# Performance work log

Hardware: AMD Instinct MI355X
Metric: run time of the kernel (lower is better)

The kernel has to match this reference:

```python
import jax, jax.numpy as jnp
import numpy as np

N = 8192       # num_nodes
DEG = 16       # edges per node
E = N * DEG    # num_edges
F = 128        # num_features
R = 20         # num_rbf_features
L = 3          # num_message_passing_layers
CUT = 3.0      # cutoff_dist


def setup_inputs() -> dict:
    key = jax.random.key(0)
    ks = jax.random.split(key, 18)
    atoms = jax.random.randint(ks[0], (N,), 1, 119)
    # every node appears as a destination exactly DEG times -> bincount > 0
    idx_i = jnp.repeat(jnp.arange(N), DEG)
    idx_j = jax.random.randint(ks[1], (E,), 0, N)
    raw = jax.random.normal(ks[2], (E, 3), jnp.float32)
    rel_dir = raw / jnp.linalg.norm(raw, axis=-1, keepdims=True)
    rel_dist = jax.random.uniform(ks[3], (E,), jnp.float32, 0.1, CUT - 1e-3)
    emb = (jax.random.normal(ks[4], (119, F), jnp.float32) / np.sqrt(F)).at[0].set(0.0)
    def w(k, shape, fan_in):
        return jax.random.normal(k, shape, jnp.float32) / np.sqrt(fan_in)
    return {
        'atoms': atoms, 'idx_i': idx_i, 'idx_j': idx_j,
        'rel_dir': rel_dir, 'rel_dist': rel_dist, 'emb': emb,
        'msg_w1': w(ks[5], (L, F, F), F), 'msg_b1': jnp.zeros((L, F), jnp.float32),
        'msg_w2': w(ks[6], (L, F, 3 * F), F), 'msg_b2': jnp.zeros((L, 3 * F), jnp.float32),
        'rbf_w': w(ks[7], (L, R, 3 * F), R), 'rbf_b': jnp.zeros((L, 3 * F), jnp.float32),
        'Uw': w(ks[8], (L, F, F), F), 'Vw': w(ks[9], (L, F, F), F),
        'upd_w1': w(ks[10], (L, 2 * F, F), 2 * F), 'upd_b1': jnp.zeros((L, F), jnp.float32),
        'upd_w2': w(ks[11], (L, F, 3 * F), F), 'upd_b2': jnp.zeros((L, 3 * F), jnp.float32),
    }


def painn_forward(atoms, idx_i, idx_j, rel_dir, rel_dist, emb,
                  msg_w1, msg_b1, msg_w2, msg_b2, rbf_w, rbf_b,
                  Uw, Vw, upd_w1, upd_b1, upd_w2, upd_b2):
    silu = jax.nn.silu
    # cosine cutoff and sinusoidal RBF features of edge distances
    cut = 0.5 * (jnp.cos(jnp.pi * rel_dist / CUT) + 1.0)               # [E]
    n = jnp.arange(1, R + 1, dtype=rel_dist.dtype)
    rbf = jnp.sin(n * jnp.pi * rel_dist[:, None] / CUT) / rel_dist[:, None]  # [E,R]

    s = emb[atoms]                                   # [N,F]
    v = jnp.zeros((N, F, 3), s.dtype)                # [N,F,3]
    counts = jax.ops.segment_sum(jnp.ones(E, s.dtype), idx_i, num_segments=N)  # bincount

    for l in range(L):
        # ---- message block ----
        phi = silu(s @ msg_w1[l] + msg_b1[l]) @ msg_w2[l] + msg_b2[l]  # [N,3F]
        W = (rbf @ rbf_w[l] + rbf_b[l]) * cut[:, None]                 # [E,3F]
        phi_W = phi[idx_j] * W                                         # [E,3F]
        p_vv, p_ss, p_vs = jnp.split(phi_W, 3, axis=-1)
        ds = jax.ops.segment_sum(p_ss, idx_i, num_segments=N) / counts[:, None]
        ve = v[idx_j] * p_vv[..., None] + p_vs[..., None] * rel_dir[:, None, :]  # [E,F,3]
        dv = jax.ops.segment_sum(ve, idx_i, num_segments=N) / counts[:, None, None]
        s = s + ds
        v = v + dv
        # ---- update block ----
        Uv = jnp.einsum('nfc,fg->ngc', v, Uw[l])       # [N,F,3]
        Vv = jnp.einsum('nfc,fg->ngc', v, Vw[l])       # [N,F,3]
        a_in = jnp.concatenate([jnp.linalg.norm(Vv, axis=-1), s], axis=-1)  # [N,2F]
        a = silu(a_in @ upd_w1[l] + upd_b1[l]) @ upd_w2[l] + upd_b2[l]      # [N,3F]
        a_vv, a_sv, a_ss = jnp.split(a, 3, axis=-1)
        s = s + a_ss + a_sv * jnp.sum(Uv * Vv, axis=-1)
        v = v + Uv * a_vv[..., None]
    return s, v


def reference(atoms, idx_i, idx_j, rel_dir, rel_dist, emb,
              msg_w1, msg_b1, msg_w2, msg_b2, rbf_w, rbf_b,
              Uw, Vw, upd_w1, upd_b1, upd_w2, upd_b2):
    return painn_forward(atoms, idx_i, idx_j, rel_dir, rel_dist, emb,
                         msg_w1, msg_b1, msg_w2, msg_b2, rbf_w, rbf_b,
                         Uw, Vw, upd_w1, upd_b1, upd_w2, upd_b2)
```

## Files before the change

### kernel.cpp

```cpp
#include <hip/hip_runtime.h>
#include <hip/hip_fp16.h>

#define N_NODES 8192
#define DEG     16
#define NEDGE   (N_NODES*DEG)
#define F       128
#define F3      384
#define RBF     20
#define NLAYER  3
#define NF      (N_NODES*F)
#define PI_F    3.14159265358979f

typedef unsigned short u16;
typedef __bf16 bf16x8 __attribute__((ext_vector_type(8)));
typedef float  f32x4  __attribute__((ext_vector_type(4)));

__device__ __forceinline__ float bf2f(u16 u){ return __uint_as_float(((unsigned)u)<<16); }
__device__ __forceinline__ u16 f2bf(float f){
  unsigned x = __float_as_uint(f);
  unsigned r = (x + 0x7FFFu + ((x>>16)&1u)) >> 16;
  return (u16)r;
}
__device__ __forceinline__ float lo_bf(unsigned u){ return __uint_as_float(u<<16); }
__device__ __forceinline__ float hi_bf(unsigned u){ return __uint_as_float(u & 0xFFFF0000u); }
__device__ __forceinline__ float silu_f(float x){ return x / (1.f + __expf(-x)); }
__device__ __forceinline__ float ldsrc(const void* src, int i, int bf){
  return bf ? bf2f(((const u16*)src)[i]) : ((const float*)src)[i];
}
__device__ __forceinline__ unsigned packh2(float a, float b){
  return (unsigned)__half_as_ushort(__float2half(a)) |
         ((unsigned)__half_as_ushort(__float2half(b)) << 16);
}
__device__ __forceinline__ __half2 u2h2(unsigned u){ return __builtin_bit_cast(__half2, u); }

__global__ void k_detect(const u16* __restrict__ rd, int* __restrict__ flag){
  if (threadIdx.x == 0 && blockIdx.x == 0){
    int ok = 1;
    for (int i = 0; i < 128; i++){
      float v = bf2f(rd[2*i]);
      if (!(v > 0.01f && v < 4.0f)) { ok = 0; break; }
    }
    *flag = ok;
  }
}

__device__ __forceinline__ void splitw(const void* src, u16* bh, u16* bl,
                                       int i, int K, int Ncol, int bf){
  int kn = K*Ncol; int l = i/kn; int r = i - l*kn; int k = r/Ncol; int n = r - k*Ncol;
  float w = ldsrc(src, i, bf);
  u16 h = f2bf(w);
  size_t o = (size_t)l*kn + (size_t)n*K + k;
  bh[o] = h; bl[o] = f2bf(w - bf2f(h));
}

__global__ __launch_bounds__(256) void k_prep(
    const void* mb1, const void* mb2, const void* b1, const void* b2,
    const void* rw,  const void* rb,
    const void* mw1, const void* mw2, const void* w1, const void* w2,
    const void* Uw,  const void* Vw,
    const void* dist, const void* dirv, const int* __restrict__ idxj,
    const int* __restrict__ atoms, const void* __restrict__ emb,
    float* c_mb1, float* c_mb2, float* c_b1, float* c_b2,
    unsigned* rwp2,
    u16* mw1h, u16* mw1l, u16* mw2h, u16* mw2l, u16* w1h, u16* w1l,
    u16* w2h, u16* w2l, u16* uvh, u16* uvl,
    uint4* edata,
    float* s, u16* s_h, u16* s_l,
    u16* p0h, u16* p0l, u16* bufA16, u16* bufB16,
    const int* __restrict__ flag){
  int i = blockIdx.x*256 + threadIdx.x;
  int bf = *flag;
  const int S0=NLAYER*F, S1=NLAYER*F3, S2=NLAYER*F, S3=NLAYER*F3;
  const int S4=NLAYER*11*F3;
  const int S5=NLAYER*F*F, S6=NLAYER*F*F3, S7=NLAYER*2*F*F, S8=NLAYER*F*F3, S9=NLAYER*256*F;
  if (i < S0){ c_mb1[i]=ldsrc(mb1,i,bf); return; } i-=S0;
  if (i < S1){ c_mb2[i]=ldsrc(mb2,i,bf); return; } i-=S1;
  if (i < S2){ c_b1[i] =ldsrc(b1, i,bf); return; } i-=S2;
  if (i < S3){ c_b2[i] =ldsrc(b2, i,bf); return; } i-=S3;
  if (i < S4){
    int l = i/(11*F3); int r = i - l*(11*F3); int r2 = r/F3; int col = r - r2*F3;
    float w0, w1v;
    if (r2 < 10){
      w0  = ldsrc(rw, (l*RBF + 2*r2  )*F3 + col, bf);
      w1v = ldsrc(rw, (l*RBF + 2*r2+1)*F3 + col, bf);
    } else {
      w0  = ldsrc(rb, l*F3 + col, bf);
      w1v = 0.f;
    }
    rwp2[i] = packh2(w0, w1v);
    return;
  } i-=S4;
  if (i < S5){ splitw(mw1, mw1h, mw1l, i, F,   F,  bf); return; } i-=S5;
  if (i < S6){ splitw(mw2, mw2h, mw2l, i, F,   F3, bf); return; } i-=S6;
  if (i < S7){ splitw(w1,  w1h,  w1l,  i, 2*F, F,  bf); return; } i-=S7;
  if (i < S8){ splitw(w2,  w2h,  w2l,  i, F,   F3, bf); return; } i-=S8;
  if (i < S9){
    int l=i/(256*F); int r=i-l*(256*F); int n=r>>7; int k=r&127;
    int si=(l*F+k)*F+(n&127);
    float w = ldsrc((n<128)?Uw:Vw, si, bf);
    u16 h=f2bf(w); uvh[i]=h; uvl[i]=f2bf(w-bf2f(h));
    return;
  } i-=S9;
  if (i < NEDGE){
    int e = i;
    float d = ldsrc(dist, e, bf);
    float cut = 0.5f*(cosf(PI_F*d*(1.f/3.f)) + 1.0f);
    float ic = cut/d;
    unsigned o[16];
    #pragma unroll
    for (int r2=0;r2<10;r2++){
      float s0 = sinf((2*r2+1)*PI_F*d*(1.f/3.f))*ic;
      float s1 = sinf((2*r2+2)*PI_F*d*(1.f/3.f))*ic;
      o[r2] = packh2(s0, s1);
    }
    o[10] = packh2(cut, 0.f);
    o[11] = __float_as_uint(ldsrc(dirv, e*3+0, bf));
    o[12] = __float_as_uint(ldsrc(dirv, e*3+1, bf));
    o[13] = __float_as_uint(ldsrc(dirv, e*3+2, bf));
    o[14] = (unsigned)idxj[e];
    o[15] = 0;
    uint4* dst = edata + (size_t)e*4;
    dst[0] = make_uint4(o[0],o[1],o[2],o[3]);
    dst[1] = make_uint4(o[4],o[5],o[6],o[7]);
    dst[2] = make_uint4(o[8],o[9],o[10],o[11]);
    dst[3] = make_uint4(o[12],o[13],o[14],o[15]);
    return;
  } i-=NEDGE;
  if (i < NF){
    int n = i >> 7, f = i & 127;
    float sv = ldsrc(emb, atoms[n]*F + f, bf);
    s[i] = sv;
    u16 hb = f2bf(sv); s_h[i] = hb; s_l[i] = f2bf(sv - bf2f(hb));
    p0h[i]=0; p0h[NF+i]=0; p0h[2*(size_t)NF+i]=0;
    p0l[i]=0; p0l[NF+i]=0; p0l[2*(size_t)NF+i]=0;
    bufA16[(size_t)i*4+2]=0; bufA16[(size_t)i*4+3]=0;
    bufB16[(size_t)i*2+1]=0;
  }
}
#define PREP_TOTAL (NLAYER*(F+F3+F+F3+11*F3+F*F+F*F3+2*F*F+F*F3+256*F) + NEDGE + NF)

__global__ __launch_bounds__(256) void k_msg(const u16* __restrict__ s_h,
                                             const u16* __restrict__ s_l,
                                             const u16* __restrict__ w1h_,
                                             const u16* __restrict__ w1l_,
                                             const u16* __restrict__ w2h_,
                                             const u16* __restrict__ w2l_,
                                             const float* __restrict__ b1,
                                             const float* __restrict__ b2,
                                             u16* __restrict__ bufA16,
                                             u16* __restrict__ bufB16){
  __shared__ u16 Ah[16*136], Al[16*136];
  __shared__ u16 Hh[16*136], Hl[16*136];
  __shared__ u16 Bh[64*136], Bl[64*136];
  int t = threadIdx.x, lane = t&63, w = t>>6;
  int row0 = blockIdx.x<<4;
  int l15 = lane&15, q8 = (lane>>4)<<3, qrow = (lane>>4)<<2;

  #pragma unroll
  for (int q=0;q<2;q++){
    int id = t + 256*q; int pl = id>>8, rem = id&255, r = rem>>4, c = (rem&15)<<3;
    *(uint4*)((pl?Al:Ah)+r*136+c) = *(const uint4*)((pl?s_l:s_h) + (size_t)(row0+r)*F + c);
  }

  for (int cg=0;cg<2;cg++){
    __syncthreads();
    #pragma unroll
    for (int q=0;q<8;q++){
      int id = t + 256*q; int pl = id>>10, rem = id&1023, r = rem>>4, c = (rem&15)<<3;
      *(uint4*)((pl?Bl:Bh)+r*136+c) = *(const uint4*)((pl?w1l_:w1h_) + (size_t)(cg*64+r)*F + c);
    }
    __syncthreads();
    f32x4 acc; acc[0]=0;acc[1]=0;acc[2]=0;acc[3]=0;
    #pragma unroll
    for (int k0=0;k0<F;k0+=32){
      bf16x8 a_h = *(const bf16x8*)&Ah[l15*136 + k0 + q8];
      bf16x8 a_l = *(const bf16x8*)&Al[l15*136 + k0 + q8];
      bf16x8 b_h = *(const bf16x8*)&Bh[(w*16+l15)*136 + k0 + q8];
      bf16x8 b_l = *(const bf16x8*)&Bl[(w*16+l15)*136 + k0 + q8];
      acc = __builtin_amdgcn_mfma_f32_16x16x32_bf16(a_h, b_h, acc, 0,0,0);
      acc = __builtin_amdgcn_mfma_f32_16x16x32_bf16(a_h, b_l, acc, 0,0,0);
      acc = __builtin_amdgcn_mfma_f32_16x16x32_bf16(a_l, b_h, acc, 0,0,0);
    }
    int col = cg*64 + w*16 + l15;
    float bb = b1[col];
    #pragma unroll
    for (int r=0;r<4;r++){
      float val = silu_f(acc[r] + bb);
      u16 hb = f2bf(val);
      Hh[(qrow+r)*136 + col] = hb;
      Hl[(qrow+r)*136 + col] = f2bf(val - bf2f(hb));
    }
  }

  for (int cg=0;cg<6;cg++){
    __syncthreads();
    #pragma unroll
    for (int q=0;q<8;q++){
      int id = t + 256*q; int pl = id>>10, rem = id&1023, r = rem>>4, c = (rem&15)<<3;
      *(uint4*)((pl?Bl:Bh)+r*136+c) = *(const uint4*)((pl?w2l_:w2h_) + (size_t)(cg*64+r)*F + c);
    }
    __syncthreads();
    f32x4 acc; acc[0]=0;acc[1]=0;acc[2]=0;acc[3]=0;
    #pragma unroll
    for (int k0=0;k0<F;k0+=32){
      bf16x8 a_h = *(const bf16x8*)&Hh[l15*136 + k0 + q8];
      bf16x8 a_l = *(const bf16x8*)&Hl[l15*136 + k0 + q8];
      bf16x8 b_h = *(const bf16x8*)&Bh[(w*16+l15)*136 + k0 + q8];
      bf16x8 b_l = *(const bf16x8*)&Bl[(w*16+l15)*136 + k0 + q8];
      acc = __builtin_amdgcn_mfma_f32_16x16x32_bf16(a_h, b_h, acc, 0,0,0);
      acc = __builtin_amdgcn_mfma_f32_16x16x32_bf16(a_h, b_l, acc, 0,0,0);
      acc = __builtin_amdgcn_mfma_f32_16x16x32_bf16(a_l, b_h, acc, 0,0,0);
    }
    int gc = cg*64 + w*16 + l15;
    float bb = b2[gc];
    #pragma unroll
    for (int r=0;r<4;r++){
      int grow = row0 + qrow + r;
      u16 v = f2bf(acc[r] + bb);
      size_t rowo = (size_t)grow*F;
      if (gc < F)        bufA16[(rowo + gc)*4 + 0]     = v;
      else if (gc < 2*F) bufA16[(rowo + gc - F)*4 + 1] = v;
      else               bufB16[(rowo + gc - 2*F)*2]   = v;
    }
  }
}

__global__ __launch_bounds__(256) void k_agg(const uint4* __restrict__ ed_g,
                                             const uint2* __restrict__ bufA,
                                             const unsigned* __restrict__ bufB,
                                             const unsigned* __restrict__ rwp2,
                                             const u16* __restrict__ vi_h,
                                             const u16* __restrict__ vi_l,
                                             u16* __restrict__ vo_h,
                                             u16* __restrict__ vo_l,
                                             float* __restrict__ s,
                                             u16* __restrict__ s_h,
                                             u16* __restrict__ s_l){
  __shared__ uint4 ed4[128];
  int t = threadIdx.x;
  int half = t >> 7, f = t & 127;

  __half2 rw2[3][11];
  #pragma unroll
  for (int r2=0;r2<11;r2++){
    rw2[0][r2] = u2h2(rwp2[r2*F3 + f]);
    rw2[1][r2] = u2h2(rwp2[r2*F3 + F + f]);
    rw2[2][r2] = u2h2(rwp2[r2*F3 + 2*F + f]);
  }

  int nA = blockIdx.x * 2;
  if (t < 128) ed4[t] = ed_g[(size_t)nA*64 + t];
  __syncthreads();

  int n = nA + half;
  int base = half*64;
  float ds=0.f, dv0=0.f, dv1=0.f, dv2=0.f;

  int j0 = (int)(ed4[base+3].z & (N_NODES-1));
  uint2    pa = bufA[(size_t)j0*F + f];
  unsigned pb = bufB[(size_t)j0*F + f];
  for (int el=0;el<DEG;el++){
    uint2 cpa = pa; unsigned cpb = pb;
    if (el+1 < DEG){
      int j1 = (int)(ed4[base+(el+1)*4+3].z & (N_NODES-1));
      pa = bufA[(size_t)j1*F + f];
      pb = bufB[(size_t)j1*F + f];
    }
    uint4 q0 = ed4[base+el*4+0];
    uint4 q1 = ed4[base+el*4+1];
    uint4 q2 = ed4[base+el*4+2];
    uint4 q3 = ed4[base+el*4+3];
    __half2 rc[11] = {u2h2(q0.x),u2h2(q0.y),u2h2(q0.z),u2h2(q0.w),
                      u2h2(q1.x),u2h2(q1.y),u2h2(q1.z),u2h2(q1.w),
                      u2h2(q2.x),u2h2(q2.y),u2h2(q2.z)};
    __half2 a0 = __hmul2(rc[0], rw2[0][0]);
    __half2 a1 = __hmul2(rc[0], rw2[1][0]);
    __half2 a2 = __hmul2(rc[0], rw2[2][0]);
    #pragma unroll
    for (int r2=1;r2<11;r2++){
      a0 = __hfma2(rc[r2], rw2[0][r2], a0);
      a1 = __hfma2(rc[r2], rw2[1][r2], a1);
      a2 = __hfma2(rc[r2], rw2[2][r2], a2);
    }
    float Wvv = __low2float(a0) + __high2float(a0);
    float Wss = __low2float(a1) + __high2float(a1);
    float Wvs = __low2float(a2) + __high2float(a2);
    float pvv = Wvv*lo_bf(cpa.x), pss = Wss*hi_bf(cpa.x), pvs = Wvs*lo_bf(cpb);
    ds += pss;
    dv0 += lo_bf(cpa.y)*pvv + pvs*__uint_as_float(q2.w);
    dv1 += hi_bf(cpa.y)*pvv + pvs*__uint_as_float(q3.x);
    dv2 += hi_bf(cpb)  *pvv + pvs*__uint_as_float(q3.y);
  }
  size_t i = (size_t)n*F + f;
  const float inv = 1.f/DEG;
  float sv = s[i] + ds*inv;
  s[i] = sv;
  { u16 hb = f2bf(sv); s_h[i] = hb; s_l[i] = f2bf(sv - bf2f(hb)); }
  float o0 = bf2f(vi_h[i])            + bf2f(vi_l[i])            + dv0*inv;
  float o1 = bf2f(vi_h[NF+i])         + bf2f(vi_l[NF+i])         + dv1*inv;
  float o2 = bf2f(vi_h[2*(size_t)NF+i]) + bf2f(vi_l[2*(size_t)NF+i]) + dv2*inv;
  u16 h0=f2bf(o0), h1=f2bf(o1), h2=f2bf(o2);
  vo_h[i]=h0; vo_h[NF+i]=h1; vo_h[2*(size_t)NF+i]=h2;
  vo_l[i]=f2bf(o0-bf2f(h0)); vo_l[NF+i]=f2bf(o1-bf2f(h1)); vo_l[2*(size_t)NF+i]=f2bf(o2-bf2f(h2));
}

__global__ __launch_bounds__(256) void k_uvdot(const u16* __restrict__ voh,
                                               const u16* __restrict__ vol,
                                               const u16* __restrict__ Bh_g,
                                               const u16* __restrict__ Bl_g,
                                               const float* __restrict__ s,
                                               float* __restrict__ uvF,
                                               float* __restrict__ dot,
                                               u16* __restrict__ ai_h,
                                               u16* __restrict__ ai_l){
  __shared__ u16 Ah[32*40], Al[32*40], BUh[64*40], BUl[64*40], BVh[64*40], BVl[64*40];
  int t = threadIdx.x;
  int row0 = blockIdx.y<<5, c0 = blockIdx.x<<6;
  int lane = t&63, w = t>>6;
  int qr = (w>>1)<<4, qc = (w&1)<<5;
  int l15 = lane&15, q8 = (lane>>4)<<3;
  int qrow = (lane>>4)<<2;
  int ap = t>>7, arem = t&127, ar = arem>>2, ac = (arem&3)<<3;
  f32x4 dA[2], nA2[2];
  dA[0][0]=0;dA[0][1]=0;dA[0][2]=0;dA[0][3]=0; dA[1]=dA[0];
  nA2[0]=dA[0]; nA2[1]=dA[0];

  for (int c=0;c<3;c++){
    f32x4 aU[2], aV[2];
    aU[0][0]=0;aU[0][1]=0;aU[0][2]=0;aU[0][3]=0; aU[1]=aU[0];
    aV[0]=aU[0]; aV[1]=aU[0];
    const u16* Asrc = (ap ? vol : voh) + (size_t)c*NF + (size_t)(row0+ar)*F + ac;
    u16* Adst = (ap ? Al : Ah) + ar*40 + ac;
    for (int k0=0;k0<F;k0+=32){
      *(uint4*)Adst = *(const uint4*)(Asrc + k0);
      #pragma unroll
      for (int q=0;q<4;q++){
        int idx = t + 256*q;
        int bp = idx>>8, rem = idx&255, br = rem>>2, bc = (rem&3)<<3;
        int grow = ((bp>>1) ? 128 : 0) + c0 + br;
        const u16* Bsrc = ((bp&1) ? Bl_g : Bh_g) + (size_t)grow*F + k0 + bc;
        u16* Bdst;
        if (bp==0) Bdst = BUh; else if (bp==1) Bdst = BUl; else if (bp==2) Bdst = BVh; else Bdst = BVl;
        *(uint4*)(Bdst + br*40 + bc) = *(const uint4*)Bsrc;
      }
      __syncthreads();
      bf16x8 a_h = *(const bf16x8*)&Ah[(qr+l15)*40 + q8];
      bf16x8 a_l = *(const bf16x8*)&Al[(qr+l15)*40 + q8];
      #pragma unroll
      for (int nt=0;nt<2;nt++){
        int off = (qc+nt*16+l15)*40 + q8;
        bf16x8 bu_h = *(const bf16x8*)&BUh[off];
        bf16x8 bu_l = *(const bf16x8*)&BUl[off];
        bf16x8 bv_h = *(const bf16x8*)&BVh[off];
        bf16x8 bv_l = *(const bf16x8*)&BVl[off];
        aU[nt] = __builtin_amdgcn_mfma_f32_16x16x32_bf16(a_h, bu_h, aU[nt], 0,0,0);
        aU[nt] = __builtin_amdgcn_mfma_f32_16x16x32_bf16(a_h, bu_l, aU[nt], 0,0,0);
        aU[nt] = __builtin_amdgcn_mfma_f32_16x16x32_bf16(a_l, bu_h, aU[nt], 0,0,0);
        aV[nt] = __builtin_amdgcn_mfma_f32_16x16x32_bf16(a_h, bv_h, aV[nt], 0,0,0);
        aV[nt] = __builtin_amdgcn_mfma_f32_16x16x32_bf16(a_h, bv_l, aV[nt], 0,0,0);
        aV[nt] = __builtin_amdgcn_mfma_f32_16x16x32_bf16(a_l, bv_h, aV[nt], 0,0,0);
      }
      __syncthreads();
    }
    #pragma unroll
    for (int nt=0;nt<2;nt++){
      int gcol = c0 + qc + nt*16 + l15;
      #pragma unroll
      for (int r=0;r<4;r++){
        int grow = row0 + qr + qrow + r;
        float u = aU[nt][r], v = aV[nt][r];
        dA[nt][r] += u*v;
        nA2[nt][r] += v*v;
        uvF[(size_t)c*NF + (size_t)grow*F + gcol] = u;
      }
    }
  }
  #pragma unroll
  for (int nt=0;nt<2;nt++){
    int gcol = c0 + qc + nt*16 + l15;
    #pragma unroll
    for (int r=0;r<4;r++){
      int grow = row0 + qr + qrow + r;
      dot[(size_t)grow*F + gcol] = dA[nt][r];
      float vn = sqrtf(nA2[nt][r]);
      float sv = s[(size_t)grow*F + gcol];
      size_t b = (size_t)grow*256 + gcol;
      u16 h0 = f2bf(vn), h1 = f2bf(sv);
      ai_h[b] = h0;     ai_l[b] = f2bf(vn - bf2f(h0));
      ai_h[b+128] = h1; ai_l[b+128] = f2bf(sv - bf2f(h1));
    }
  }
}

__global__ __launch_bounds__(256) void k_upd(const u16* __restrict__ ai_h,
                                             const u16* __restrict__ ai_l,
                                             const u16* __restrict__ w1h_,
                                             const u16* __restrict__ w1l_,
                                             const u16* __restrict__ w2h_,
                                             const u16* __restrict__ w2l_,
                                             const float* __restrict__ b1,
                                             const float* __restrict__ b2,
                                             const float* __restrict__ dot,
                                             const float* __restrict__ uvF,
                                             float* __restrict__ s,
                                             u16* __restrict__ s_h,
                                             u16* __restrict__ s_l,
                                             u16* __restrict__ v_h,
                                             u16* __restrict__ v_l,
                                             u16* __restrict__ bufA16,
                                             u16* __restrict__ bufB16,
                                             float* __restrict__ out){
  __shared__ u16 Ah[16*264], Al[16*264];
  __shared__ u16 Hh[16*136], Hl[16*136];
  __shared__ u16 Bh[64*136], Bl[64*136];
  __shared__ __half aLDS[16*392];
  int t = threadIdx.x, lane = t&63, w = t>>6;
  int row0 = blockIdx.x<<4;
  int l15 = lane&15, q8 = (lane>>4)<<3, qrow = (lane>>4)<<2;

  #pragma unroll
  for (int q=0;q<4;q++){
    int id = t + 256*q; int pl = id>>9, rem = id&511, r = rem>>5, c = (rem&31)<<3;
    *(uint4*)((pl?Al:Ah)+r*264+c) = *(const uint4*)((pl?ai_l:ai_h) + (size_t)(row0+r)*256 + c);
  }

  for (int cg=0;cg<2;cg++){
    f32x4 acc; acc[0]=0;acc[1]=0;acc[2]=0;acc[3]=0;
    for (int kc=0;kc<4;kc++){
      __syncthreads();
      #pragma unroll
      for (int q=0;q<4;q++){
        int id = t + 256*q; int pl = id>>9, rem = id&511, r = rem>>3, c = (rem&7)<<3;
        *(uint4*)((pl?Bl:Bh)+r*136+c) =
            *(const uint4*)((pl?w1l_:w1h_) + (size_t)(cg*64+r)*256 + kc*64 + c);
      }
      __syncthreads();
      #pragma unroll
      for (int ks=0;ks<64;ks+=32){
        bf16x8 a_h = *(const bf16x8*)&Ah[l15*264 + kc*64 + ks + q8];
        bf16x8 a_l = *(const bf16x8*)&Al[l15*264 + kc*64 + ks + q8];
        bf16x8 b_h = *(const bf16x8*)&Bh[(w*16+l15)*136 + ks + q8];
        bf16x8 b_l = *(const bf16x8*)&Bl[(w*16+l15)*136 + ks + q8];
        acc = __builtin_amdgcn_mfma_f32_16x16x32_bf16(a_h, b_h, acc, 0,0,0);
        acc = __builtin_amdgcn_mfma_f32_16x16x32_bf16(a_h, b_l, acc, 0,0,0);
        acc = __builtin_amdgcn_mfma_f32_16x16x32_bf16(a_l, b_h, acc, 0,0,0);
      }
    }
    int col = cg*64 + w*16 + l15;
    float bb = b1[col];
    #pragma unroll
    for (int r=0;r<4;r++){
      float val = silu_f(acc[r] + bb);
      u16 hb = f2bf(val);
      Hh[(qrow+r)*136 + col] = hb;
      Hl[(qrow+r)*136 + col] = f2bf(val - bf2f(hb));
    }
  }

  for (int cg=0;cg<6;cg++){
    __syncthreads();
    #pragma unroll
    for (int q=0;q<8;q++){
      int id = t + 256*q; int pl = id>>10, rem = id&1023, r = rem>>4, c = (rem&15)<<3;
      *(uint4*)((pl?Bl:Bh)+r*136+c) = *(const uint4*)((pl?w2l_:w2h_) + (size_t)(cg*64+r)*F + c);
    }
    __syncthreads();
    f32x4 acc; acc[0]=0;acc[1]=0;acc[2]=0;acc[3]=0;
    #pragma unroll
    for (int k0=0;k0<F;k0+=32){
      bf16x8 a_h = *(const bf16x8*)&Hh[l15*136 + k0 + q8];
      bf16x8 a_l = *(const bf16x8*)&Hl[l15*136 + k0 + q8];
      bf16x8 b_h = *(const bf16x8*)&Bh[(w*16+l15)*136 + k0 + q8];
      bf16x8 b_l = *(const bf16x8*)&Bl[(w*16+l15)*136 + k0 + q8];
      acc = __builtin_amdgcn_mfma_f32_16x16x32_bf16(a_h, b_h, acc, 0,0,0);
      acc = __builtin_amdgcn_mfma_f32_16x16x32_bf16(a_h, b_l, acc, 0,0,0);
      acc = __builtin_amdgcn_mfma_f32_16x16x32_bf16(a_l, b_h, acc, 0,0,0);
    }
    int gc = cg*64 + w*16 + l15;
    float bb = b2[gc];
    #pragma unroll
    for (int r=0;r<4;r++)
      aLDS[(qrow+r)*392 + gc] = __float2half(acc[r] + bb);
  }
  __syncthreads();

  int f = t & 127, rh = (t>>7)*8;
  #pragma unroll
  for (int e=0;e<8;e++){
    int r = rh + e;
    int grow = row0 + r;
    size_t i = (size_t)grow*F + f;
    float avv = __half2float(aLDS[r*392 + f]);
    float asv = __half2float(aLDS[r*392 + F + f]);
    float ass = __half2float(aLDS[r*392 + 2*F + f]);
    float sv = s[i] + ass + asv*dot[i];
    s[i] = sv;
    u16 hb = f2bf(sv); s_h[i] = hb; s_l[i] = f2bf(sv - bf2f(hb));
    float nv0 = bf2f(v_h[i])              + bf2f(v_l[i])              + uvF[i]*avv;
    float nv1 = bf2f(v_h[NF+i])           + bf2f(v_l[NF+i])           + uvF[NF+i]*avv;
    float nv2 = bf2f(v_h[2*(size_t)NF+i]) + bf2f(v_l[2*(size_t)NF+i]) + uvF[2*(size_t)NF+i]*avv;
    u16 h0=f2bf(nv0), h1=f2bf(nv1), h2=f2bf(nv2);
    v_h[i]=h0; v_h[NF+i]=h1; v_h[2*(size_t)NF+i]=h2;
    v_l[i]=f2bf(nv0-bf2f(h0)); v_l[NF+i]=f2bf(nv1-bf2f(h1)); v_l[2*(size_t)NF+i]=f2bf(nv2-bf2f(h2));
    bufA16[(size_t)i*4+2] = h0; bufA16[(size_t)i*4+3] = h1;
    bufB16[(size_t)i*2+1] = h2;
    if (out){
      out[i] = sv;
      out[NF + (size_t)i*3 + 0] = nv0;
      out[NF + (size_t)i*3 + 1] = nv1;
      out[NF + (size_t)i*3 + 2] = nv2;
    }
  }
}

extern "C" void kernel_launch(void* const* d_in, const int* in_sizes, int n_in,
                              void* d_out, int out_size, void* d_ws, size_t ws_size,
                              hipStream_t stream) {
  const int* atoms   = (const int*)d_in[0];
  const int* idxj    = (const int*)d_in[2];

  float* W = (float*)d_ws;
  size_t off = 64;
  int* flag = (int*)d_ws;
  #define ALLOCF(name, cnt) float* name = W+off; off += (((cnt)+63)&~(size_t)63)
  #define ALLOCU(name, cnt) u16* name = (u16*)(W+off); off += ((((cnt)+1)/2+63)&~(size_t)63)
  ALLOCF(c_mb1, NLAYER*F);
  ALLOCF(c_mb2, NLAYER*F3);
  ALLOCF(c_b1,  NLAYER*F);
  ALLOCF(c_b2,  NLAYER*F3);
  unsigned* c_rwp2 = (unsigned*)(W+off); off += ((NLAYER*11*F3+63)&~(size_t)63);
  uint4* edata = (uint4*)(W+off); off += (size_t)NEDGE*16;
  ALLOCU(w_mw1h, NLAYER*F*F);   ALLOCU(w_mw1l, NLAYER*F*F);
  ALLOCU(w_mw2h, NLAYER*F*F3);  ALLOCU(w_mw2l, NLAYER*F*F3);
  ALLOCU(w_uvh,  NLAYER*256*F); ALLOCU(w_uvl,  NLAYER*256*F);
  ALLOCU(w_w1h,  NLAYER*F*256); ALLOCU(w_w1l,  NLAYER*F*256);
  ALLOCU(w_w2h,  NLAYER*F*F3);  ALLOCU(w_w2l,  NLAYER*F*F3);
  uint2* bufA = (uint2*)(W+off); off += (size_t)2*NF;
  unsigned* bufB = (unsigned*)(W+off); off += (size_t)NF;
  ALLOCU(p0h, (size_t)3*NF); ALLOCU(p0l, (size_t)3*NF);
  ALLOCU(p1h, (size_t)3*NF); ALLOCU(p1l, (size_t)3*NF);
  ALLOCU(s_h,  NF); ALLOCU(s_l,  NF);
  ALLOCU(ai_h, (size_t)2*NF); ALLOCU(ai_l, (size_t)2*NF);
  ALLOCF(s,    NF);
  ALLOCF(uvF,  (size_t)3*NF);
  ALLOCF(dotb, NF);

  k_detect<<<1, 64, 0, stream>>>((const u16*)d_in[4], flag);
  k_prep<<<(PREP_TOTAL+255)/256, 256, 0, stream>>>(
      d_in[7], d_in[9], d_in[15], d_in[17],
      d_in[10], d_in[11],
      d_in[6], d_in[8], d_in[14], d_in[16],
      d_in[12], d_in[13],
      d_in[4], d_in[3], idxj,
      atoms, d_in[5],
      c_mb1, c_mb2, c_b1, c_b2, c_rwp2,
      w_mw1h, w_mw1l, w_mw2h, w_mw2l, w_w1h, w_w1l,
      w_w2h, w_w2l, w_uvh, w_uvl, edata,
      s, s_h, s_l, p0h, p0l, (u16*)bufA, (u16*)bufB, flag);

  for (int l=0; l<NLAYER; l++){
    u16* vih = (l & 1) ? p1h : p0h;
    u16* vil = (l & 1) ? p1l : p0l;
    u16* voh = (l & 1) ? p0h : p1h;
    u16* vol = (l & 1) ? p0l : p1l;
    k_msg<<<N_NODES/16, 256, 0, stream>>>(
        s_h, s_l,
        w_mw1h + (size_t)l*F*F,  w_mw1l + (size_t)l*F*F,
        w_mw2h + (size_t)l*F*F3, w_mw2l + (size_t)l*F*F3,
        c_mb1 + (size_t)l*F, c_mb2 + (size_t)l*F3,
        (u16*)bufA, (u16*)bufB);
    k_agg<<<N_NODES/2, 256, 0, stream>>>(
        edata, bufA, bufB, c_rwp2 + (size_t)l*11*F3,
        vih, vil, voh, vol, s, s_h, s_l);
    k_uvdot<<<dim3(2, N_NODES/32), 256, 0, stream>>>(
        voh, vol, w_uvh + (size_t)l*256*F, w_uvl + (size_t)l*256*F,
        s, uvF, dotb, ai_h, ai_l);
    k_upd<<<N_NODES/16, 256, 0, stream>>>(
        ai_h, ai_l,
        w_w1h + (size_t)l*F*256, w_w1l + (size_t)l*F*256,
        w_w2h + (size_t)l*F*F3,  w_w2l + (size_t)l*F*F3,
        c_b1 + (size_t)l*F, c_b2 + (size_t)l*F3,
        dotb, uvF, s, s_h, s_l, voh, vol,
        (u16*)bufA, (u16*)bufB,
        (l == NLAYER-1) ? (float*)d_out : nullptr);
  }
}
```

Baseline: 388.5 us.

## Compute RBF edge filters with MFMA into LDS instead of per-thread half2 FMAs

```diff
diff --git a/kernel.cpp b/kernel.cpp
--- a/kernel.cpp
+++ b/kernel.cpp
@@ -27,11 +27,6 @@
 __device__ __forceinline__ float ldsrc(const void* src, int i, int bf){
   return bf ? bf2f(((const u16*)src)[i]) : ((const float*)src)[i];
 }
-__device__ __forceinline__ unsigned packh2(float a, float b){
-  return (unsigned)__half_as_ushort(__float2half(a)) |
-         ((unsigned)__half_as_ushort(__float2half(b)) << 16);
-}
-__device__ __forceinline__ __half2 u2h2(unsigned u){ return __builtin_bit_cast(__half2, u); }
 
 __global__ void k_detect(const u16* __restrict__ rd, int* __restrict__ flag){
   if (threadIdx.x == 0 && blockIdx.x == 0){
@@ -61,35 +56,23 @@
     const void* dist, const void* dirv, const int* __restrict__ idxj,
     const int* __restrict__ atoms, const void* __restrict__ emb,
     float* c_mb1, float* c_mb2, float* c_b1, float* c_b2,
-    unsigned* rwp2,
     u16* mw1h, u16* mw1l, u16* mw2h, u16* mw2l, u16* w1h, u16* w1l,
     u16* w2h, u16* w2l, u16* uvh, u16* uvl,
-    uint4* edata,
+    u16* rwB,
+    u16* ed_rc,
+    uint4* ed2,
     float* s, u16* s_h, u16* s_l,
     u16* p0h, u16* p0l, u16* bufA16, u16* bufB16,
     const int* __restrict__ flag){
   int i = blockIdx.x*256 + threadIdx.x;
   int bf = *flag;
   const int S0=NLAYER*F, S1=NLAYER*F3, S2=NLAYER*F, S3=NLAYER*F3;
-  const int S4=NLAYER*11*F3;
   const int S5=NLAYER*F*F, S6=NLAYER*F*F3, S7=NLAYER*2*F*F, S8=NLAYER*F*F3, S9=NLAYER*256*F;
+  const int SB=NLAYER*24*64*8;
   if (i < S0){ c_mb1[i]=ldsrc(mb1,i,bf); return; } i-=S0;
   if (i < S1){ c_mb2[i]=ldsrc(mb2,i,bf); return; } i-=S1;
   if (i < S2){ c_b1[i] =ldsrc(b1, i,bf); return; } i-=S2;
   if (i < S3){ c_b2[i] =ldsrc(b2, i,bf); return; } i-=S3;
-  if (i < S4){
-    int l = i/(11*F3); int r = i - l*(11*F3); int r2 = r/F3; int col = r - r2*F3;
-    float w0, w1v;
-    if (r2 < 10){
-      w0  = ldsrc(rw, (l*RBF + 2*r2  )*F3 + col, bf);
-      w1v = ldsrc(rw, (l*RBF + 2*r2+1)*F3 + col, bf);
-    } else {
-      w0  = ldsrc(rb, l*F3 + col, bf);
-      w1v = 0.f;
-    }
-    rwp2[i] = packh2(w0, w1v);
-    return;
-  } i-=S4;
   if (i < S5){ splitw(mw1, mw1h, mw1l, i, F,   F,  bf); return; } i-=S5;
   if (i < S6){ splitw(mw2, mw2h, mw2l, i, F,   F3, bf); return; } i-=S6;
   if (i < S7){ splitw(w1,  w1h,  w1l,  i, 2*F, F,  bf); return; } i-=S7;
@@ -101,29 +84,35 @@
     u16 h=f2bf(w); uvh[i]=h; uvl[i]=f2bf(w-bf2f(h));
     return;
   } i-=S9;
+  if (i < SB){
+    int l = i/12288; int r = i - l*12288;
+    int nt = r>>9; int rem = r&511; int lane = rem>>3; int j = rem&7;
+    int k = ((lane>>4)<<3) + j; int n = nt*16 + (lane&15);
+    float v;
+    if (k < RBF)       v = ldsrc(rw, (l*RBF + k)*F3 + n, bf);
+    else if (k == RBF) v = ldsrc(rb, l*F3 + n, bf);
+    else               v = 0.f;
+    rwB[i] = f2bf(v);
+    return;
+  } i-=SB;
   if (i < NEDGE){
-    int e = i;
+    int e = i; int n = e>>4; int el = e&15;
     float d = ldsrc(dist, e, bf);
     float cut = 0.5f*(cosf(PI_F*d*(1.f/3.f)) + 1.0f);
     float ic = cut/d;
-    unsigned o[16];
-    #pragma unroll
-    for (int r2=0;r2<10;r2++){
-      float s0 = sinf((2*r2+1)*PI_F*d*(1.f/3.f))*ic;
-      float s1 = sinf((2*r2+2)*PI_F*d*(1.f/3.f))*ic;
-      o[r2] = packh2(s0, s1);
-    }
-    o[10] = packh2(cut, 0.f);
-    o[11] = __float_as_uint(ldsrc(dirv, e*3+0, bf));
-    o[12] = __float_as_uint(ldsrc(dirv, e*3+1, bf));
-    o[13] = __float_as_uint(ldsrc(dirv, e*3+2, bf));
-    o[14] = (unsigned)idxj[e];
-    o[15] = 0;
-    uint4* dst = edata + (size_t)e*4;
-    dst[0] = make_uint4(o[0],o[1],o[2],o[3]);
-    dst[1] = make_uint4(o[4],o[5],o[6],o[7]);
-    dst[2] = make_uint4(o[8],o[9],o[10],o[11]);
-    dst[3] = make_uint4(o[12],o[13],o[14],o[15]);
+    u16* dst = ed_rc + (size_t)n*512;
+    #pragma unroll
+    for (int k=0;k<32;k++){
+      float v;
+      if (k < RBF)       v = sinf((k+1)*PI_F*d*(1.f/3.f))*ic;
+      else if (k == RBF) v = cut;
+      else               v = 0.f;
+      dst[(((k>>3)<<4) + el)*8 + (k&7)] = f2bf(v);
+    }
+    ed2[e] = make_uint4(__float_as_uint(ldsrc(dirv,e*3+0,bf)),
+                        __float_as_uint(ldsrc(dirv,e*3+1,bf)),
+                        __float_as_uint(ldsrc(dirv,e*3+2,bf)),
+                        (unsigned)idxj[e]);
     return;
   } i-=NEDGE;
   if (i < NF){
@@ -137,7 +126,7 @@
     bufB16[(size_t)i*2+1]=0;
   }
 }
-#define PREP_TOTAL (NLAYER*(F+F3+F+F3+11*F3+F*F+F*F3+2*F*F+F*F3+256*F) + NEDGE + NF)
+#define PREP_TOTAL (NLAYER*(F+F3+F+F3+F*F+F*F3+2*F*F+F*F3+256*F+24*64*8) + NEDGE + NF)
 
 __global__ __launch_bounds__(256) void k_msg(const u16* __restrict__ s_h,
                                              const u16* __restrict__ s_l,
@@ -225,10 +214,11 @@
   }
 }
 
-__global__ __launch_bounds__(256) void k_agg(const uint4* __restrict__ ed_g,
+__global__ __launch_bounds__(256) void k_agg(const u16* __restrict__ ed_rc,
+                                             const uint4* __restrict__ ed2,
+                                             const u16* __restrict__ rwB,
                                              const uint2* __restrict__ bufA,
                                              const unsigned* __restrict__ bufB,
-                                             const unsigned* __restrict__ rwp2,
                                              const u16* __restrict__ vi_h,
                                              const u16* __restrict__ vi_l,
                                              u16* __restrict__ vo_h,
@@ -236,72 +226,69 @@
                                              float* __restrict__ s,
                                              u16* __restrict__ s_h,
                                              u16* __restrict__ s_l){
-  __shared__ uint4 ed4[128];
-  int t = threadIdx.x;
-  int half = t >> 7, f = t & 127;
-
-  __half2 rw2[3][11];
-  #pragma unroll
-  for (int r2=0;r2<11;r2++){
-    rw2[0][r2] = u2h2(rwp2[r2*F3 + f]);
-    rw2[1][r2] = u2h2(rwp2[r2*F3 + F + f]);
-    rw2[2][r2] = u2h2(rwp2[r2*F3 + 2*F + f]);
-  }
-
-  int nA = blockIdx.x * 2;
-  if (t < 128) ed4[t] = ed_g[(size_t)nA*64 + t];
+  __shared__ u16 Wt[F3*66];
+  __shared__ uint4 e2[64];
+  int t = threadIdx.x, lane = t&63, w = t>>6;
+  int n0 = blockIdx.x<<2;
+
+  if (t < 64) e2[t] = ed2[(size_t)n0*DEG + t];
+
+  bf16x8 a = *(const bf16x8*)(ed_rc + ((size_t)(n0+w))*512 + lane*8);
+  int fl = lane&15;
+  int colw = (w<<4) + ((lane>>4)<<2);
+  #pragma unroll 4
+  for (int nt=0;nt<24;nt++){
+    bf16x8 b = *(const bf16x8*)(rwB + ((nt<<6) + lane)*8);
+    f32x4 dacc; dacc[0]=0.f; dacc[1]=0.f; dacc[2]=0.f; dacc[3]=0.f;
+    dacc = __builtin_amdgcn_mfma_f32_16x16x32_bf16(a, b, dacc, 0,0,0);
+    int f = (nt<<4) + fl;
+    unsigned lo = (unsigned)f2bf(dacc[0]) | ((unsigned)f2bf(dacc[1])<<16);
+    unsigned hi = (unsigned)f2bf(dacc[2]) | ((unsigned)f2bf(dacc[3])<<16);
+    *(unsigned*)&Wt[f*66 + colw]     = lo;
+    *(unsigned*)&Wt[f*66 + colw + 2] = hi;
+  }
   __syncthreads();
 
-  int n = nA + half;
-  int base = half*64;
-  float ds=0.f, dv0=0.f, dv1=0.f, dv2=0.f;
-
-  int j0 = (int)(ed4[base+3].z & (N_NODES-1));
-  uint2    pa = bufA[(size_t)j0*F + f];
-  unsigned pb = bufB[(size_t)j0*F + f];
-  for (int el=0;el<DEG;el++){
-    uint2 cpa = pa; unsigned cpb = pb;
-    if (el+1 < DEG){
-      int j1 = (int)(ed4[base+(el+1)*4+3].z & (N_NODES-1));
-      pa = bufA[(size_t)j1*F + f];
-      pb = bufB[(size_t)j1*F + f];
-    }
-    uint4 q0 = ed4[base+el*4+0];
-    uint4 q1 = ed4[base+el*4+1];
-    uint4 q2 = ed4[base+el*4+2];
-    uint4 q3 = ed4[base+el*4+3];
-    __half2 rc[11] = {u2h2(q0.x),u2h2(q0.y),u2h2(q0.z),u2h2(q0.w),
-                      u2h2(q1.x),u2h2(q1.y),u2h2(q1.z),u2h2(q1.w),
-                      u2h2(q2.x),u2h2(q2.y),u2h2(q2.z)};
-    __half2 a0 = __hmul2(rc[0], rw2[0][0]);
-    __half2 a1 = __hmul2(rc[0], rw2[1][0]);
-    __half2 a2 = __hmul2(rc[0], rw2[2][0]);
-    #pragma unroll
-    for (int r2=1;r2<11;r2++){
-      a0 = __hfma2(rc[r2], rw2[0][r2], a0);
-      a1 = __hfma2(rc[r2], rw2[1][r2], a1);
-      a2 = __hfma2(rc[r2], rw2[2][r2], a2);
-    }
-    float Wvv = __low2float(a0) + __high2float(a0);
-    float Wss = __low2float(a1) + __high2float(a1);
-    float Wvs = __low2float(a2) + __high2float(a2);
-    float pvv = Wvv*lo_bf(cpa.x), pss = Wss*hi_bf(cpa.x), pvs = Wvs*lo_bf(cpb);
-    ds += pss;
-    dv0 += lo_bf(cpa.y)*pvv + pvs*__uint_as_float(q2.w);
-    dv1 += hi_bf(cpa.y)*pvv + pvs*__uint_as_float(q3.x);
-    dv2 += hi_bf(cpb)  *pvv + pvs*__uint_as_float(q3.y);
-  }
-  size_t i = (size_t)n*F + f;
   const float inv = 1.f/DEG;
-  float sv = s[i] + ds*inv;
-  s[i] = sv;
-  { u16 hb = f2bf(sv); s_h[i] = hb; s_l[i] = f2bf(sv - bf2f(hb)); }
-  float o0 = bf2f(vi_h[i])            + bf2f(vi_l[i])            + dv0*inv;
-  float o1 = bf2f(vi_h[NF+i])         + bf2f(vi_l[NF+i])         + dv1*inv;
-  float o2 = bf2f(vi_h[2*(size_t)NF+i]) + bf2f(vi_l[2*(size_t)NF+i]) + dv2*inv;
-  u16 h0=f2bf(o0), h1=f2bf(o1), h2=f2bf(o2);
-  vo_h[i]=h0; vo_h[NF+i]=h1; vo_h[2*(size_t)NF+i]=h2;
-  vo_l[i]=f2bf(o0-bf2f(h0)); vo_l[NF+i]=f2bf(o1-bf2f(h1)); vo_l[2*(size_t)NF+i]=f2bf(o2-bf2f(h2));
+  for (int p=0;p<2;p++){
+    int nl = (p<<1) + (t>>7);
+    int n  = n0 + nl;
+    int f  = t & 127;
+    float ds=0.f, dv0=0.f, dv1=0.f, dv2=0.f;
+    int j0 = (int)(e2[nl*DEG].w & (N_NODES-1));
+    uint2 pa = bufA[(size_t)j0*F + f];
+    unsigned pb = bufB[(size_t)j0*F + f];
+    const u16* Wvv_p = &Wt[f*66 + nl*DEG];
+    const u16* Wss_p = &Wt[(F+f)*66 + nl*DEG];
+    const u16* Wvs_p = &Wt[(2*F+f)*66 + nl*DEG];
+    for (int el=0; el<DEG; el++){
+      uint2 cpa=pa; unsigned cpb=pb;
+      if (el+1 < DEG){
+        int j1 = (int)(e2[nl*DEG+el+1].w & (N_NODES-1));
+        pa = bufA[(size_t)j1*F + f];
+        pb = bufB[(size_t)j1*F + f];
+      }
+      float Wvv = bf2f(Wvv_p[el]);
+      float Wss = bf2f(Wss_p[el]);
+      float Wvs = bf2f(Wvs_p[el]);
+      uint4 q = e2[nl*DEG + el];
+      float pvv = Wvv*lo_bf(cpa.x), pss = Wss*hi_bf(cpa.x), pvs = Wvs*lo_bf(cpb);
+      ds += pss;
+      dv0 += lo_bf(cpa.y)*pvv + pvs*__uint_as_float(q.x);
+      dv1 += hi_bf(cpa.y)*pvv + pvs*__uint_as_float(q.y);
+      dv2 += hi_bf(cpb)  *pvv + pvs*__uint_as_float(q.z);
+    }
+    size_t i = (size_t)n*F + f;
+    float sv = s[i] + ds*inv;
+    s[i] = sv;
+    u16 hb = f2bf(sv); s_h[i] = hb; s_l[i] = f2bf(sv - bf2f(hb));
+    float o0 = bf2f(vi_h[i])              + bf2f(vi_l[i])              + dv0*inv;
+    float o1 = bf2f(vi_h[NF+i])           + bf2f(vi_l[NF+i])           + dv1*inv;
+    float o2 = bf2f(vi_h[2*(size_t)NF+i]) + bf2f(vi_l[2*(size_t)NF+i]) + dv2*inv;
+    u16 h0=f2bf(o0), h1=f2bf(o1), h2=f2bf(o2);
+    vo_h[i]=h0; vo_h[NF+i]=h1; vo_h[2*(size_t)NF+i]=h2;
+    vo_l[i]=f2bf(o0-bf2f(h0)); vo_l[NF+i]=f2bf(o1-bf2f(h1)); vo_l[2*(size_t)NF+i]=f2bf(o2-bf2f(h2));
+  }
 }
 
 __global__ __launch_bounds__(256) void k_uvdot(const u16* __restrict__ voh,
@@ -528,8 +515,9 @@
   ALLOCF(c_mb2, NLAYER*F3);
   ALLOCF(c_b1,  NLAYER*F);
   ALLOCF(c_b2,  NLAYER*F3);
-  unsigned* c_rwp2 = (unsigned*)(W+off); off += ((NLAYER*11*F3+63)&~(size_t)63);
-  uint4* edata = (uint4*)(W+off); off += (size_t)NEDGE*16;
+  ALLOCU(w_rwB, NLAYER*24*64*8);
+  ALLOCU(ed_rc, (size_t)N_NODES*512);
+  uint4* e2g = (uint4*)(W+off); off += (size_t)NEDGE*4;
   ALLOCU(w_mw1h, NLAYER*F*F);   ALLOCU(w_mw1l, NLAYER*F*F);
   ALLOCU(w_mw2h, NLAYER*F*F3);  ALLOCU(w_mw2l, NLAYER*F*F3);
   ALLOCU(w_uvh,  NLAYER*256*F); ALLOCU(w_uvl,  NLAYER*256*F);
@@ -553,9 +541,10 @@
       d_in[12], d_in[13],
       d_in[4], d_in[3], idxj,
       atoms, d_in[5],
-      c_mb1, c_mb2, c_b1, c_b2, c_rwp2,
+      c_mb1, c_mb2, c_b1, c_b2,
       w_mw1h, w_mw1l, w_mw2h, w_mw2l, w_w1h, w_w1l,
-      w_w2h, w_w2l, w_uvh, w_uvl, edata,
+      w_w2h, w_w2l, w_uvh, w_uvl,
+      w_rwB, ed_rc, e2g,
       s, s_h, s_l, p0h, p0l, (u16*)bufA, (u16*)bufB, flag);
 
   for (int l=0; l<NLAYER; l++){
@@ -569,9 +558,9 @@
         w_mw2h + (size_t)l*F*F3, w_mw2l + (size_t)l*F*F3,
         c_mb1 + (size_t)l*F, c_mb2 + (size_t)l*F3,
         (u16*)bufA, (u16*)bufB);
-    k_agg<<<N_NODES/2, 256, 0, stream>>>(
-        edata, bufA, bufB, c_rwp2 + (size_t)l*11*F3,
-        vih, vil, voh, vol, s, s_h, s_l);
+    k_agg<<<N_NODES/4, 256, 0, stream>>>(
+        ed_rc, e2g, w_rwB + (size_t)l*12288,
+        bufA, bufB, vih, vil, voh, vol, s, s_h, s_l);
     k_uvdot<<<dim3(2, N_NODES/32), 256, 0, stream>>>(
         voh, vol, w_uvh + (size_t)l*256*F, w_uvl + (size_t)l*256*F,
         s, uvF, dotb, ai_h, ai_l);
```

Result: slower. 444.6 us (+14.4%).
